# Optimization experiments

Measured on AMD Instinct MI355X. Metric: run time of the kernel, lower is better.

## Reference

```python
import jax, jax.numpy as jnp
import numpy as np
from jax import lax

B, T, L, OUT, SP, E, H = 128, 300, 28, 28, 7, 20, 256
W = T - L + 1          # 273 sliding windows
W_OUT = W - OUT        # 245 training windows
F_IN = L + 1 + E       # 49 rnn input features


def _lstm_dilated(x, d, Wih, Whh, b):
    # x: [T0, B, F]; dilation d realized by phase-stacking time into batch (zalando DRNN scheme)
    T0, Bn, F = x.shape
    pad = (-T0) % d
    if pad:
        x = jnp.concatenate([x, jnp.zeros((pad, Bn, F), x.dtype)], axis=0)
    Tn = x.shape[0] // d
    xd = x.reshape(Tn, d * Bn, F)  # element [k, j*Bn:(j+1)*Bn] == x[k*d+j]
    Hh = Whh.shape[1]

    def step(carry, xt):
        h, c = carry
        z = xt @ Wih.T + h @ Whh.T + b
        i, f, g, o = jnp.split(z, 4, axis=-1)  # torch LSTM gate order i,f,g,o
        c = jax.nn.sigmoid(f) * c + jax.nn.sigmoid(i) * jnp.tanh(g)
        h = jax.nn.sigmoid(o) * jnp.tanh(c)
        return (h, c), h

    h0 = jnp.zeros((d * Bn, Hh), x.dtype)
    _, hs = lax.scan(step, (h0, h0), xd)
    return hs.reshape(Tn * d, Bn, Hh)[:T0]


def _forward(train_dataset, val_dataset, alpha_raw, gamma_raw, init_seas,
             input_categories, my_param,
             Wih1, Whh1, b1, Wih2, Whh2, b2, Wih3, Whh3, b3, Wih4, Whh4, b4,
             linear_W, linear_b, score_W, score_b):
    x = train_dataset
    a = jax.nn.sigmoid(alpha_raw)   # [B]
    g = jax.nn.sigmoid(gamma_raw)   # [B]
    S0 = jnp.exp(init_seas)         # [B,7] = seasonalities[0..6]
    s7 = S0[:, 0]                   # seasonalities[7] = exp(init[:,0])
    level0 = x[:, 0] / S0[:, 0]
    buf0 = jnp.concatenate([S0[:, 1:], s7[:, None]], axis=1)  # S[1..7], shift register

    def es_step(carry, xt):
        level, buf = carry
        s = buf[:, 0]
        lvl = a * (xt / s) + (1.0 - a) * level
        s_new = g * (xt / lvl) + (1.0 - g) * s
        buf = jnp.concatenate([buf[:, 1:], s_new[:, None]], axis=1)
        return (lvl, buf), (lvl, s_new)

    _, (lvls, s_news) = lax.scan(es_step, (level0, buf0), x[:, 1:].T)
    levels = jnp.concatenate([level0[None], lvls], axis=0).T        # [B,T]
    S_full = jnp.concatenate([S0, s7[:, None], s_news.T], axis=1)   # [B,T+7]
    # extension: cat(S_full, S_full[:, T : T-7+28])  -> [B, T+28]
    S_ext = jnp.concatenate([S_full, S_full[:, T:T - SP + OUT]], axis=1)

    # input windows (vectorized over all W window positions)
    widx = jnp.arange(W)[:, None] + jnp.arange(L)[None, :]          # [W,L]
    lvl_w = levels[:, L - 1 + jnp.arange(W)]                        # [B,W]
    norm_in = x[:, widx] / S_ext[:, widx] / lvl_w[:, :, None]       # [B,W,L]
    cats = jnp.broadcast_to(input_categories[:, None, :], (B, W, E))
    cat_in = jnp.concatenate([norm_in, cats], axis=2)[jnp.arange(B) % 10]  # original j%10 row pick
    mp = jnp.broadcast_to(my_param.reshape(1, 1, 1), (B, W, 1))
    window_input = jnp.transpose(jnp.concatenate([cat_in, mp], axis=2), (1, 0, 2))  # [W,B,F_IN]

    # output windows
    oidx = (L + jnp.arange(W_OUT))[:, None] + jnp.arange(OUT)[None, :]  # [W_OUT,OUT]
    lvl_o = levels[:, L - 1 + jnp.arange(W_OUT)]                        # [B,W_OUT]
    window_output = jnp.transpose(x[:, oidx] / S_ext[:, oidx] / lvl_o[:, :, None], (1, 0, 2))

    # residual dilated LSTM stack: block1 dilations (1,2); block2 dilations (2,6) + residual
    h1 = _lstm_dilated(window_input, 1, Wih1, Whh1, b1)
    h1 = _lstm_dilated(h1, 2, Wih2, Whh2, b2)
    h2 = _lstm_dilated(h1, 2, Wih3, Whh3, b3)
    h2 = _lstm_dilated(h2, 6, Wih4, Whh4, b4) + h1
    h = jnp.tanh(h2 @ linear_W.T + linear_b)
    rnn_out = h @ score_W.T + score_b                                   # [W,B,OUT]

    # LSTM stack is causal, so running on window_input[:-OUT] equals slicing the full run
    prediction_values = rnn_out[:-OUT]
    actual_values = window_output
    holdout = rnn_out[-1] * S_ext[:, -OUT:] * levels[:, -1:]
    holdout_prediction = holdout * (holdout > 0).astype(holdout.dtype)
    hav = val_dataset
    hav_norm = hav / S_ext[:, -OUT:] / levels[:, -1:]
    return (prediction_values, actual_values, holdout_prediction, rnn_out, hav, hav_norm)


def setup_inputs() -> dict:
    key = jax.random.key(0)
    ks = jax.random.split(key, 24)
    s = float(1.0 / np.sqrt(H))
    u = lambda k, shape: jax.random.uniform(k, shape, jnp.float32, -s, s)
    inp = {
        "train_dataset": jax.random.uniform(ks[0], (B, T), jnp.float32) * 2.0 + 0.5,  # positive sales
        "val_dataset": jax.random.uniform(ks[1], (B, OUT), jnp.float32) * 2.0 + 0.5,
        "alpha_raw": jnp.full((B,), 0.5, jnp.float32),
        "gamma_raw": jnp.full((B,), 0.5, jnp.float32),
        "init_seas": jnp.full((B, SP), 0.5, jnp.float32),
        "input_categories": jnp.full((B, E), 0.001, jnp.float32) + 0.01 * jax.random.normal(ks[2], (B, E), jnp.float32),
        "my_param": jnp.full((1,), 0.001, jnp.float32),
        "Wih1": u(ks[3], (4 * H, F_IN)), "Whh1": u(ks[4], (4 * H, H)), "b1": u(ks[5], (4 * H,)),
        "Wih2": u(ks[6], (4 * H, H)), "Whh2": u(ks[7], (4 * H, H)), "b2": u(ks[8], (4 * H,)),
        "Wih3": u(ks[9], (4 * H, H)), "Whh3": u(ks[10], (4 * H, H)), "b3": u(ks[11], (4 * H,)),
        "Wih4": u(ks[12], (4 * H, H)), "Whh4": u(ks[13], (4 * H, H)), "b4": u(ks[14], (4 * H,)),
        "linear_W": u(ks[15], (H, H)), "linear_b": u(ks[16], (H,)),
        "score_W": u(ks[17], (OUT, H)), "score_b": u(ks[18], (OUT,)),
    }
    return inp


def reference(train_dataset, val_dataset, alpha_raw, gamma_raw, init_seas,
              input_categories, my_param,
              Wih1, Whh1, b1, Wih2, Whh2, b2, Wih3, Whh3, b3, Wih4, Whh4, b4,
              linear_W, linear_b, score_W, score_b):
    return _forward(train_dataset, val_dataset, alpha_raw, gamma_raw, init_seas,
                    input_categories, my_param,
                    Wih1, Whh1, b1, Wih2, Whh2, b2, Wih3, Whh3, b3, Wih4, Whh4, b4,
                    linear_W, linear_b, score_W, score_b)
```

## Files before the change

kernel.cpp:

```cpp
#include <hip/hip_runtime.h>

typedef unsigned short u16;
typedef unsigned int   u32;

static __device__ __forceinline__ float sigf (float x){ return 1.0f/(1.0f+__expf(-x)); }
static __device__ __forceinline__ float tanh_(float x){ return 2.0f/(1.0f+__expf(-2.0f*x)) - 1.0f; }

#define NM 2730
#define N_O0 878080
#define N_O3 978432

static __device__ __forceinline__ int dot4(u32 a, u32 b, int acc){
#if __has_builtin(__builtin_amdgcn_sdot4)
  return __builtin_amdgcn_sdot4((int)a, (int)b, acc, false);
#else
  int s = acc;
  #pragma unroll
  for(int i=0;i<4;i++){
    int av = (int)((signed char)((a >> (8*i)) & 0xffu));
    int bv = (int)((signed char)((b >> (8*i)) & 0xffu));
    s += av*bv;
  }
  return s;
#endif
}

__global__ __launch_bounds__(256) void k_prep(
    const float* __restrict__ x,     float* __restrict__ xT,
    const float* __restrict__ wi0,   float* __restrict__ wT0,
    const float* __restrict__ wi1,   float* __restrict__ wT1,
    const float* __restrict__ wi2,   float* __restrict__ wT2,
    const float* __restrict__ wi3,   float* __restrict__ wT3,
    const float* __restrict__ lw,    float* __restrict__ lwT,
    const float* __restrict__ sw,    float* __restrict__ swT,
    const float* __restrict__ h0, const float* __restrict__ h1,
    const float* __restrict__ h2, const float* __restrict__ h3,
    float* __restrict__ zsc){
  int i = blockIdx.x*256 + threadIdx.x;
  if(i < 38400){
    int t = i >> 7, b = i & 127;
    xT[i] = x[b*300 + t];
    return;
  }
  i -= 38400;
  if(i < 50176){ int c=i/1024, r=i-c*1024; wT0[i] = wi0[r*49 + c];  return; }
  i -= 50176;
  if(i < 262144){ int c=i>>10, r=i&1023; wT1[i] = wi1[r*256 + c];   return; }
  i -= 262144;
  if(i < 262144){ int c=i>>10, r=i&1023; wT2[i] = wi2[r*256 + c];   return; }
  i -= 262144;
  if(i < 262144){ int c=i>>10, r=i&1023; wT3[i] = wi3[r*256 + c];   return; }
  i -= 262144;
  if(i < 65536){ int c=i>>8, r=i&255; lwT[i] = lw[r*256 + c];       return; }
  i -= 65536;
  if(i < 7168){ int c=i/28, r=i-c*28; swT[i] = sw[r*256 + c];       return; }
  i -= 7168;
  if(i < 4096){
    int l = i >> 10, r = i & 1023;
    const float* W = (l==0)?h0:(l==1)?h1:(l==2)?h2:h3;
    const float4* p = (const float4*)(W + (size_t)r*256);
    float m = 0.f;
    #pragma unroll 8
    for(int q=0;q<64;q++){
      float4 v = p[q];
      m = fmaxf(m, fmaxf(fmaxf(fabsf(v.x),fabsf(v.y)), fmaxf(fabsf(v.z),fabsf(v.w))));
    }
    zsc[i] = fmaxf(m, 1e-20f) * (1.0f/16129.0f);
  }
}

__global__ __launch_bounds__(256) void k_packes(
    const float* __restrict__ h0, const float* __restrict__ h1,
    const float* __restrict__ h2, const float* __restrict__ h3,
    const float* __restrict__ zsc, u32* __restrict__ W8,
    const float* __restrict__ xT, const float* __restrict__ alpha,
    const float* __restrict__ gamma, const float* __restrict__ iseas,
    float* __restrict__ ST, float* __restrict__ lvlT){
  if(blockIdx.x < 1024){
    int i = blockIdx.x*256 + threadIdx.x;
    int l = i >> 16;
    int uidx = i & 65535;
    int dw = uidx & 3;
    int kg = (uidx >> 2) & 127;
    int q  = (uidx >> 9) & 3;
    int rr = (uidx >> 11) & 7;
    int js = uidx >> 14;
    int row = rr*128 + kg;
    int k0  = js*64 + q*16 + dw*4;
    const float* W = (l==0)?h0:(l==1)?h1:(l==2)?h2:h3;
    float inv = 1.0f / (zsc[l*1024 + row] * 127.0f);
    u32 out = 0;
    #pragma unroll
    for(int b=0;b<4;b++){
      float v = W[(size_t)row*256 + k0 + b];
      int q8 = max(-127, min(127, __float2int_rn(v * inv)));
      out |= ((u32)(q8 & 0xff)) << (8*b);
    }
    W8[i] = out;
    return;
  }
  int b = threadIdx.x;
  if(b >= 128) return;
  float a = sigf(alpha[b]);
  float g = sigf(gamma[b]);
  float S0[7];
  #pragma unroll
  for(int i=0;i<7;i++){ S0[i] = __expf(iseas[b*7+i]); ST[i*128+b] = S0[i]; }
  ST[7*128+b] = S0[0];
  float q0=S0[1],q1=S0[2],q2=S0[3],q3=S0[4],q4=S0[5],q5=S0[6],q6=S0[0];
  float lvl = xT[b]/S0[0];
  lvlT[b] = lvl;
  for(int t=1;t<300;t++){
    float xt = xT[t*128+b];
    float s  = q0;
    lvl = a*(xt/s) + (1.0f-a)*lvl;
    float sn = g*(xt/lvl) + (1.0f-g)*s;
    q0=q1;q1=q2;q2=q3;q3=q4;q4=q5;q5=q6;q6=sn;
    lvlT[t*128+b]   = lvl;
    ST[(t+7)*128+b] = sn;
  }
}

__global__ __launch_bounds__(256) void k_gemm1(
    const float* __restrict__ xT, const float* __restrict__ ST,
    const float* __restrict__ lvlT, const float* __restrict__ cats,
    const float* __restrict__ mp,
    const float* __restrict__ WT,
    const float* __restrict__ bias,
    float* __restrict__ Z){
  __shared__ float Xs[8][52];
  const int tid = threadIdx.x;
  const int m0 = blockIdx.x*8;
  for(int idx=tid; idx<8*49; idx+=256){
    int p = idx/49, f = idx - p*49;
    int m = m0+p;
    float v = 0.f;
    if(m < NM){
      int tt = m/10, jj = m - (m/10)*10;
      if(f < 28){
        int c = tt + f;
        v = xT[c*128 + jj] / ST[c*128 + jj] / lvlT[(tt+27)*128 + jj];
      } else if(f < 48){
        v = cats[jj*20 + (f-28)];
      } else {
        v = mp[0];
      }
    }
    Xs[p][f] = v;
  }
  __syncthreads();
  float acc0[8], acc1[8], acc2[8], acc3[8];
  {
    float b0 = bias[tid];
    float b1 = bias[tid+256];
    float b2 = bias[tid+512];
    float b3 = bias[tid+768];
    #pragma unroll
    for(int p=0;p<8;p++){ acc0[p]=b0; acc1[p]=b1; acc2[p]=b2; acc3[p]=b3; }
  }
  #pragma unroll 7
  for(int f=0; f<49; f++){
    float w0 = WT[f*1024 + tid      ];
    float w1 = WT[f*1024 + tid+256  ];
    float w2 = WT[f*1024 + tid+512  ];
    float w3 = WT[f*1024 + tid+768  ];
    #pragma unroll
    for(int p=0;p<8;p++){
      float xv = Xs[p][f];
      acc0[p] += w0*xv; acc1[p] += w1*xv; acc2[p] += w2*xv; acc3[p] += w3*xv;
    }
  }
  for(int p=0;p<8;p++){
    int m = m0+p;
    if(m < NM){
      float* zb = Z + m*1024 + tid;
      zb[0]=acc0[p]; zb[256]=acc1[p]; zb[512]=acc2[p]; zb[768]=acc3[p];
    }
  }
}

__global__ __launch_bounds__(256) void k_gemm(const float* __restrict__ X,
                                              const float* __restrict__ WT,
                                              const float* __restrict__ bias,
                                              float* __restrict__ Z){
  __shared__ float Xs[8][256];
  const int tid = threadIdx.x;
  const int m0 = blockIdx.x*8;
  for(int p=0;p<8;p++){
    int m = m0+p;
    Xs[p][tid] = (m < NM) ? X[m*256+tid] : 0.0f;
  }
  __syncthreads();
  float acc0[8], acc1[8], acc2[8], acc3[8];
  {
    float b0 = bias[tid];
    float b1 = bias[tid+256];
    float b2 = bias[tid+512];
    float b3 = bias[tid+768];
    #pragma unroll
    for(int p=0;p<8;p++){ acc0[p]=b0; acc1[p]=b1; acc2[p]=b2; acc3[p]=b3; }
  }
  #pragma unroll 4
  for(int f=0; f<256; f++){
    float w0 = WT[f*1024 + tid      ];
    float w1 = WT[f*1024 + tid+256  ];
    float w2 = WT[f*1024 + tid+512  ];
    float w3 = WT[f*1024 + tid+768  ];
    #pragma unroll
    for(int p=0;p<8;p++){
      float xv = Xs[p][f];
      acc0[p] += w0*xv; acc1[p] += w1*xv; acc2[p] += w2*xv; acc3[p] += w3*xv;
    }
  }
  for(int p=0;p<8;p++){
    int m = m0+p;
    if(m < NM){
      float* zb = Z + m*1024 + tid;
      zb[0]=acc0[p]; zb[256]=acc1[p]; zb[512]=acc2[p]; zb[768]=acc3[p];
    }
  }
}

__global__ __launch_bounds__(512) void k_scan8(
    const float* __restrict__ Z,
    const u32* __restrict__ W8,
    const float* __restrict__ zsc,
    float* __restrict__ Y,
    const float* __restrict__ RES,
    int d){
  __shared__ __align__(16) u32 h8[64];
  __shared__ int   zp[4][1024];
  __shared__ float sc[1024];
  __shared__ __align__(16) u32 wl[5*2048];
  const int tid = threadIdx.x;
  const int chain = blockIdx.x;
  const int j = chain % 10;
  const int r = chain / 10;
  const int ns = (273 - r + d - 1)/d;
  const int kg = tid & 127;
  const int js = tid >> 7;
  const uint4* Wb = (const uint4*)W8 + (size_t)js*4096 + kg;
  const uint4* hq = (const uint4*)h8 + js*4;
  uint4* wl4 = (uint4*)wl;

  for(int i=tid;i<1024;i+=512) sc[i] = zsc[i];
  #pragma unroll
  for(int rr=0;rr<5;rr++) wl4[rr*512 + tid] = Wb[rr*512];
  if(tid < 64) h8[tid] = 0u;
  float cst = 0.0f;
  __syncthreads();

  int t = r;
  for(int s=0; s<ns; s++, t+=d){
    const size_t row = (size_t)(t*10 + j);
    float zv0=0.f, zv1=0.f, zv2=0.f, zv3=0.f, rv=0.f;
    if(tid < 256){
      const float* zb = Z + row*1024;
      zv0 = zb[tid]; zv1 = zb[tid+256]; zv2 = zb[tid+512]; zv3 = zb[tid+768];
      if(RES) rv = RES[row*256 + tid];
    }
    int a0=0,a1=0,a2=0,a3=0,a4=0,a5=0,a6=0,a7=0;
    #pragma unroll
    for(int q=0;q<4;q++){
      uint4 h4 = hq[q];
      #pragma unroll
      for(int rr=0;rr<8;rr++){
        uint4 w = (q==0 && rr<5) ? wl4[rr*512 + tid] : Wb[rr*512 + q*128];
        int* ap = (rr==0)?&a0:(rr==1)?&a1:(rr==2)?&a2:(rr==3)?&a3:
                  (rr==4)?&a4:(rr==5)?&a5:(rr==6)?&a6:&a7;
        int acc = *ap;
        acc = dot4(w.x, h4.x, acc);
        acc = dot4(w.y, h4.y, acc);
        acc = dot4(w.z, h4.z, acc);
        acc = dot4(w.w, h4.w, acc);
        *ap = acc;
      }
    }
    zp[js][       kg] = a0;
    zp[js][128  + kg] = a1;
    zp[js][256  + kg] = a2;
    zp[js][384  + kg] = a3;
    zp[js][512  + kg] = a4;
    zp[js][640  + kg] = a5;
    zp[js][768  + kg] = a6;
    zp[js][896  + kg] = a7;
    __syncthreads();
    if(tid < 256){
      const int u = tid;
      int si = zp[0][u]     + zp[1][u]     + zp[2][u]     + zp[3][u];
      int sf = zp[0][u+256] + zp[1][u+256] + zp[2][u+256] + zp[3][u+256];
      int sg = zp[0][u+512] + zp[1][u+512] + zp[2][u+512] + zp[3][u+512];
      int so = zp[0][u+768] + zp[1][u+768] + zp[2][u+768] + zp[3][u+768];
      float zi = zv0 + sc[u]     * (float)si;
      float zf = zv1 + sc[u+256] * (float)sf;
      float zg = zv2 + sc[u+512] * (float)sg;
      float zo = zv3 + sc[u+768] * (float)so;
      float c  = sigf(zf)*cst + sigf(zi)*tanh_(zg);
      float h  = sigf(zo)*tanh_(c);
      cst = c;
      int hqi = __float2int_rn(h * 127.0f);
      hqi = max(-127, min(127, hqi));
      ((signed char*)h8)[u] = (signed char)hqi;
      Y[row*256 + u] = h + rv;
    }
    __syncthreads();
  }
}

__global__ __launch_bounds__(256) void k_headout(const float* __restrict__ Y4,
    const float* __restrict__ LWT,
    const float* __restrict__ lb,
    const float* __restrict__ SWT,
    const float* __restrict__ sb,
    const float* __restrict__ ST, const float* __restrict__ lvlT,
    const float* __restrict__ xT, const float* __restrict__ val,
    float* __restrict__ out){
  __shared__ float v [8][256];
  __shared__ float h2[8][256];
  const int tid = threadIdx.x;
  if(blockIdx.x >= 342){
    int i = (blockIdx.x - 342)*256 + tid;
    if(i < N_O0){
      int o = i % 28;
      int b = (i/28) % 128;
      int t = i/(28*128);
      int c = 28 + t + o;
      out[878080 + i] = xT[c*128+b] / ST[c*128+b] / lvlT[(27+t)*128+b];
    } else {
      i -= N_O0;
      if(i < 3584){
        int b = i/28, o = i%28;
        int col = (o < 21) ? (286+o) : (279+o);
        float Sm = ST[col*128 + b];
        float lv = lvlT[299*128 + b];
        out[2738176 + i] = val[i];
        out[2741760 + i] = val[i] / Sm / lv;
      }
    }
    return;
  }
  const int m0 = blockIdx.x*8;
  for(int p=0;p<8;p++){
    int m = m0+p;
    v[p][tid] = (m<NM) ? Y4[m*256+tid] : 0.0f;
  }
  __syncthreads();
  float acc[8];
  float bz = lb[tid];
  #pragma unroll
  for(int p=0;p<8;p++) acc[p]=bz;
  #pragma unroll 4
  for(int f=0; f<256; f++){
    float w = LWT[f*256+tid];
    #pragma unroll
    for(int p=0;p<8;p++) acc[p] += w * v[p][f];
  }
  #pragma unroll
  for(int p=0;p<8;p++) h2[p][tid] = tanh_(acc[p]);
  __syncthreads();
  if(tid < 224){
    int o = tid % 28, p = tid / 28;
    int m = m0 + p;
    if(m < NM){
      float a = sb[o];
      for(int f=0; f<256; f++) a += SWT[f*28+o] * h2[p][f];
      int t = m / 10, j = m - t*10;
      float* o0 = out;
      float* o3 = out + 1759744;
      for(int b=j; b<128; b+=10){
        size_t idx = (size_t)t*3584 + b*28 + o;
        o3[idx] = a;
        if(t < 245) o0[idx] = a;
      }
      if(t == 272){
        int col = (o < 21) ? (286+o) : (279+o);
        float* o2 = out + 1756160;
        for(int b=j; b<128; b+=10){
          float hv = a * ST[col*128 + b] * lvlT[299*128 + b];
          o2[b*28 + o] = (hv > 0.0f) ? hv : 0.0f;
        }
      }
    }
  }
}

extern "C" void kernel_launch(void* const* d_in, const int* in_sizes, int n_in,
                              void* d_out, int out_size, void* d_ws, size_t ws_size,
                              hipStream_t stream){
  (void)in_sizes; (void)n_in; (void)out_size; (void)ws_size;
  const float* x     = (const float*)d_in[0];
  const float* val   = (const float*)d_in[1];
  const float* alpha = (const float*)d_in[2];
  const float* gamma = (const float*)d_in[3];
  const float* iseas = (const float*)d_in[4];
  const float* cats  = (const float*)d_in[5];
  const float* mp    = (const float*)d_in[6];
  const float* Wih[4]  = {(const float*)d_in[7],  (const float*)d_in[10], (const float*)d_in[13], (const float*)d_in[16]};
  const float* Whh[4]  = {(const float*)d_in[8],  (const float*)d_in[11], (const float*)d_in[14], (const float*)d_in[17]};
  const float* bias[4] = {(const float*)d_in[9],  (const float*)d_in[12], (const float*)d_in[15], (const float*)d_in[18]};
  const float* linW  = (const float*)d_in[19];
  const float* linb  = (const float*)d_in[20];
  const float* scW   = (const float*)d_in[21];
  const float* scb   = (const float*)d_in[22];

  float* Fw   = (float*)d_ws;
  float* ST   = Fw;
  float* lvlT = ST   + 39296;
  float* xT   = lvlT + 38400;
  float* xz   = xT   + 38400;
  float* yA   = xz   + 2795520;
  float* yB   = yA   + 698880;
  float* wihT[4];
  wihT[0] = yB + 698880;
  wihT[1] = wihT[0] + 50176;
  wihT[2] = wihT[1] + 262144;
  wihT[3] = wihT[2] + 262144;
  float* linWT = wihT[3] + 262144;
  float* scT   = linWT + 65536;
  float* zsc   = scT   + 7168;
  u32*   W8all = (u32*)(zsc + 4096);

  k_prep<<<3718, 256, 0, stream>>>(x, xT,
      Wih[0], wihT[0], Wih[1], wihT[1], Wih[2], wihT[2], Wih[3], wihT[3],
      linW, linWT, scW, scT,
      Whh[0], Whh[1], Whh[2], Whh[3], zsc);

  k_packes<<<1025, 256, 0, stream>>>(Whh[0], Whh[1], Whh[2], Whh[3], zsc, W8all,
                                     xT, alpha, gamma, iseas, ST, lvlT);

  const int    dlt[4]    = {1, 2, 2, 6};
  const int    chains[4] = {10, 20, 20, 60};
  const float* Xin[4]    = {nullptr, yA, yB, yA};
  float*       Yout[4]   = {yA, yB, yA, yA};
  for(int l=0;l<4;l++){
    if(l == 0)
      k_gemm1<<<(NM+7)/8, 256, 0, stream>>>(xT, ST, lvlT, cats, mp,
                                            wihT[0], bias[0], xz);
    else
      k_gemm<<<(NM+7)/8, 256, 0, stream>>>(Xin[l], wihT[l], bias[l], xz);
    k_scan8<<<chains[l], 512, 0, stream>>>(xz, W8all + l*65536, zsc + l*1024,
                                           Yout[l],
                                           (l==3) ? yB : (const float*)nullptr, dlt[l]);
  }

  k_headout<<<342 + (N_O0 + 3584 + 255)/256, 256, 0, stream>>>(
      yA, linWT, linb, scT, scb, ST, lvlT, xT, val, (float*)d_out);
}
```

Measured before the change: 1.037 ms.

## Restructure recurrent scan to one gate row per thread with 1024 threads

The int8 recurrent matvec is remapped so each of 1024 threads computes one full gate row over all 256 hidden inputs. This removes the cross-thread partial-sum reduction through shared memory and one barrier's worth of work. The weight packing layout changes to match: 9 of the 16 k-chunks stay resident in LDS (144KB), and the other 7 are reloaded from global or L2 into registers every step. The trailing __syncthreads is replaced with a raw s_waitcnt/s_barrier, which adds register pressure and makes correctness depend on that inline asm.

```diff
diff --git a/kernel.cpp b/kernel.cpp
--- a/kernel.cpp
+++ b/kernel.cpp
@@ -79,14 +79,11 @@
   if(blockIdx.x < 1024){
     int i = blockIdx.x*256 + threadIdx.x;
     int l = i >> 16;
-    int uidx = i & 65535;
-    int dw = uidx & 3;
-    int kg = (uidx >> 2) & 127;
-    int q  = (uidx >> 9) & 3;
-    int rr = (uidx >> 11) & 7;
-    int js = uidx >> 14;
-    int row = rr*128 + kg;
-    int k0  = js*64 + q*16 + dw*4;
+    int p = i & 65535;
+    int dw  = p & 3;
+    int row = (p >> 2) & 1023;
+    int iw  = p >> 12;
+    int k0  = iw*16 + dw*4;
     const float* W = (l==0)?h0:(l==1)?h1:(l==2)?h2:h3;
     float inv = 1.0f / (zsc[l*1024 + row] * 127.0f);
     u32 out = 0;
@@ -221,31 +218,28 @@
   }
 }
 
-__global__ __launch_bounds__(512) void k_scan8(
+__global__ __launch_bounds__(1024) void k_scan8(
     const float* __restrict__ Z,
     const u32* __restrict__ W8,
     const float* __restrict__ zsc,
     float* __restrict__ Y,
     const float* __restrict__ RES,
     int d){
+  __shared__ __align__(16) u32 wl[9*4096];
   __shared__ __align__(16) u32 h8[64];
-  __shared__ int   zp[4][1024];
-  __shared__ float sc[1024];
-  __shared__ __align__(16) u32 wl[5*2048];
+  __shared__ float zf[1024];
   const int tid = threadIdx.x;
   const int chain = blockIdx.x;
   const int j = chain % 10;
   const int r = chain / 10;
   const int ns = (273 - r + d - 1)/d;
-  const int kg = tid & 127;
-  const int js = tid >> 7;
-  const uint4* Wb = (const uint4*)W8 + (size_t)js*4096 + kg;
-  const uint4* hq = (const uint4*)h8 + js*4;
+  const uint4* Wc = (const uint4*)W8;
   uint4* wl4 = (uint4*)wl;
-
-  for(int i=tid;i<1024;i+=512) sc[i] = zsc[i];
+  const uint4* hq = (const uint4*)h8;
+
   #pragma unroll
-  for(int rr=0;rr<5;rr++) wl4[rr*512 + tid] = Wb[rr*512];
+  for(int i=0;i<9;i++) wl4[i*1024 + tid] = Wc[i*1024 + tid];
+  const float sct = zsc[tid];
   if(tid < 64) h8[tid] = 0u;
   float cst = 0.0f;
   __syncthreads();
@@ -253,49 +247,53 @@
   int t = r;
   for(int s=0; s<ns; s++, t+=d){
     const size_t row = (size_t)(t*10 + j);
-    float zv0=0.f, zv1=0.f, zv2=0.f, zv3=0.f, rv=0.f;
-    if(tid < 256){
-      const float* zb = Z + row*1024;
-      zv0 = zb[tid]; zv1 = zb[tid+256]; zv2 = zb[tid+512]; zv3 = zb[tid+768];
-      if(RES) rv = RES[row*256 + tid];
-    }
-    int a0=0,a1=0,a2=0,a3=0,a4=0,a5=0,a6=0,a7=0;
-    #pragma unroll
-    for(int q=0;q<4;q++){
-      uint4 h4 = hq[q];
-      #pragma unroll
-      for(int rr=0;rr<8;rr++){
-        uint4 w = (q==0 && rr<5) ? wl4[rr*512 + tid] : Wb[rr*512 + q*128];
-        int* ap = (rr==0)?&a0:(rr==1)?&a1:(rr==2)?&a2:(rr==3)?&a3:
-                  (rr==4)?&a4:(rr==5)?&a5:(rr==6)?&a6:&a7;
-        int acc = *ap;
-        acc = dot4(w.x, h4.x, acc);
-        acc = dot4(w.y, h4.y, acc);
-        acc = dot4(w.z, h4.z, acc);
-        acc = dot4(w.w, h4.w, acc);
-        *ap = acc;
-      }
-    }
-    zp[js][       kg] = a0;
-    zp[js][128  + kg] = a1;
-    zp[js][256  + kg] = a2;
-    zp[js][384  + kg] = a3;
-    zp[js][512  + kg] = a4;
-    zp[js][640  + kg] = a5;
-    zp[js][768  + kg] = a6;
-    zp[js][896  + kg] = a7;
+    uint4 ws0 = Wc[ 9*1024 + tid];
+    uint4 ws1 = Wc[10*1024 + tid];
+    uint4 ws2 = Wc[11*1024 + tid];
+    uint4 ws3 = Wc[12*1024 + tid];
+    uint4 ws4 = Wc[13*1024 + tid];
+    uint4 ws5 = Wc[14*1024 + tid];
+    uint4 ws6 = Wc[15*1024 + tid];
+    float zv = Z[row*1024 + tid];
+    float rv = 0.f;
+    if(RES && tid < 256) rv = RES[row*256 + tid];
+
+    int acc = 0;
+    #pragma unroll
+    for(int i=0;i<9;i++){
+      uint4 w  = wl4[i*1024 + tid];
+      uint4 h4 = hq[i];
+      acc = dot4(w.x, h4.x, acc);
+      acc = dot4(w.y, h4.y, acc);
+      acc = dot4(w.z, h4.z, acc);
+      acc = dot4(w.w, h4.w, acc);
+    }
+    {
+      uint4 h4;
+      h4 = hq[ 9]; acc = dot4(ws0.x,h4.x,acc); acc = dot4(ws0.y,h4.y,acc);
+                   acc = dot4(ws0.z,h4.z,acc); acc = dot4(ws0.w,h4.w,acc);
+      h4 = hq[10]; acc = dot4(ws1.x,h4.x,acc); acc = dot4(ws1.y,h4.y,acc);
+                   acc = dot4(ws1.z,h4.z,acc); acc = dot4(ws1.w,h4.w,acc);
+      h4 = hq[11]; acc = dot4(ws2.x,h4.x,acc); acc = dot4(ws2.y,h4.y,acc);
+                   acc = dot4(ws2.z,h4.z,acc); acc = dot4(ws2.w,h4.w,acc);
+      h4 = hq[12]; acc = dot4(ws3.x,h4.x,acc); acc = dot4(ws3.y,h4.y,acc);
+                   acc = dot4(ws3.z,h4.z,acc); acc = dot4(ws3.w,h4.w,acc);
+      h4 = hq[13]; acc = dot4(ws4.x,h4.x,acc); acc = dot4(ws4.y,h4.y,acc);
+                   acc = dot4(ws4.z,h4.z,acc); acc = dot4(ws4.w,h4.w,acc);
+      h4 = hq[14]; acc = dot4(ws5.x,h4.x,acc); acc = dot4(ws5.y,h4.y,acc);
+                   acc = dot4(ws5.z,h4.z,acc); acc = dot4(ws5.w,h4.w,acc);
+      h4 = hq[15]; acc = dot4(ws6.x,h4.x,acc); acc = dot4(ws6.y,h4.y,acc);
+                   acc = dot4(ws6.z,h4.z,acc); acc = dot4(ws6.w,h4.w,acc);
+    }
+    zf[tid] = zv + sct * (float)acc;
     __syncthreads();
     if(tid < 256){
       const int u = tid;
-      int si = zp[0][u]     + zp[1][u]     + zp[2][u]     + zp[3][u];
-      int sf = zp[0][u+256] + zp[1][u+256] + zp[2][u+256] + zp[3][u+256];
-      int sg = zp[0][u+512] + zp[1][u+512] + zp[2][u+512] + zp[3][u+512];
-      int so = zp[0][u+768] + zp[1][u+768] + zp[2][u+768] + zp[3][u+768];
-      float zi = zv0 + sc[u]     * (float)si;
-      float zf = zv1 + sc[u+256] * (float)sf;
-      float zg = zv2 + sc[u+512] * (float)sg;
-      float zo = zv3 + sc[u+768] * (float)so;
-      float c  = sigf(zf)*cst + sigf(zi)*tanh_(zg);
+      float zi = zf[u];
+      float zff= zf[u+256];
+      float zg = zf[u+512];
+      float zo = zf[u+768];
+      float c  = sigf(zff)*cst + sigf(zi)*tanh_(zg);
       float h  = sigf(zo)*tanh_(c);
       cst = c;
       int hqi = __float2int_rn(h * 127.0f);
@@ -303,7 +301,7 @@
       ((signed char*)h8)[u] = (signed char)hqi;
       Y[row*256 + u] = h + rv;
     }
-    __syncthreads();
+    asm volatile("s_waitcnt lgkmcnt(0)\n\ts_barrier" ::: "memory");
   }
 }
 
@@ -438,9 +436,9 @@
                                             wihT[0], bias[0], xz);
     else
       k_gemm<<<(NM+7)/8, 256, 0, stream>>>(Xin[l], wihT[l], bias[l], xz);
-    k_scan8<<<chains[l], 512, 0, stream>>>(xz, W8all + l*65536, zsc + l*1024,
-                                           Yout[l],
-                                           (l==3) ? yB : (const float*)nullptr, dlt[l]);
+    k_scan8<<<chains[l], 1024, 0, stream>>>(xz, W8all + l*65536, zsc + l*1024,
+                                            Yout[l],
+                                            (l==3) ? yB : (const float*)nullptr, dlt[l]);
   }
 
   k_headout<<<342 + (N_O0 + 3584 + 255)/256, 256, 0, stream>>>(
```

After: 1.104 ms. 1.07x slower.

## Fuse all stages into one cooperative persistent kernel with grid syncs

Applied to the files above, without the earlier changes.

Replaces the sequence of prep, pack, gemm, scan and head kernel launches with a single cooperative kernel of 256 blocks that runs every stage and uses grid-wide barriers between them. It also drops the LDS-cached weight preload in the scan and loads the ES input series into shared memory for the serial smoothing loop. The aim is to remove the launch and inter-kernel gaps across the many small stages. In exchange, the gemm stages run on only 256 blocks with 512 threads using a single large static LDS buffer, so occupancy and gemm throughput may drop, and grid sync has its own cost.

```diff
diff --git a/kernel.cpp b/kernel.cpp
--- a/kernel.cpp
+++ b/kernel.cpp
@@ -1,14 +1,14 @@
 #include <hip/hip_runtime.h>
-
-typedef unsigned short u16;
-typedef unsigned int   u32;
+#include <hip/hip_cooperative_groups.h>
+namespace cg = cooperative_groups;
+
+typedef unsigned int u32;
 
 static __device__ __forceinline__ float sigf (float x){ return 1.0f/(1.0f+__expf(-x)); }
 static __device__ __forceinline__ float tanh_(float x){ return 2.0f/(1.0f+__expf(-2.0f*x)) - 1.0f; }
 
 #define NM 2730
 #define N_O0 878080
-#define N_O3 978432
 
 static __device__ __forceinline__ int dot4(u32 a, u32 b, int acc){
 #if __has_builtin(__builtin_amdgcn_sdot4)
@@ -25,227 +25,100 @@
 #endif
 }
 
-__global__ __launch_bounds__(256) void k_prep(
-    const float* __restrict__ x,     float* __restrict__ xT,
-    const float* __restrict__ wi0,   float* __restrict__ wT0,
-    const float* __restrict__ wi1,   float* __restrict__ wT1,
-    const float* __restrict__ wi2,   float* __restrict__ wT2,
-    const float* __restrict__ wi3,   float* __restrict__ wT3,
-    const float* __restrict__ lw,    float* __restrict__ lwT,
-    const float* __restrict__ sw,    float* __restrict__ swT,
-    const float* __restrict__ h0, const float* __restrict__ h1,
-    const float* __restrict__ h2, const float* __restrict__ h3,
-    float* __restrict__ zsc){
-  int i = blockIdx.x*256 + threadIdx.x;
-  if(i < 38400){
-    int t = i >> 7, b = i & 127;
-    xT[i] = x[b*300 + t];
-    return;
-  }
-  i -= 38400;
-  if(i < 50176){ int c=i/1024, r=i-c*1024; wT0[i] = wi0[r*49 + c];  return; }
-  i -= 50176;
-  if(i < 262144){ int c=i>>10, r=i&1023; wT1[i] = wi1[r*256 + c];   return; }
-  i -= 262144;
-  if(i < 262144){ int c=i>>10, r=i&1023; wT2[i] = wi2[r*256 + c];   return; }
-  i -= 262144;
-  if(i < 262144){ int c=i>>10, r=i&1023; wT3[i] = wi3[r*256 + c];   return; }
-  i -= 262144;
-  if(i < 65536){ int c=i>>8, r=i&255; lwT[i] = lw[r*256 + c];       return; }
-  i -= 65536;
-  if(i < 7168){ int c=i/28, r=i-c*28; swT[i] = sw[r*256 + c];       return; }
-  i -= 7168;
-  if(i < 4096){
-    int l = i >> 10, r = i & 1023;
-    const float* W = (l==0)?h0:(l==1)?h1:(l==2)?h2:h3;
-    const float4* p = (const float4*)(W + (size_t)r*256);
-    float m = 0.f;
-    #pragma unroll 8
-    for(int q=0;q<64;q++){
-      float4 v = p[q];
-      m = fmaxf(m, fmaxf(fmaxf(fabsf(v.x),fabsf(v.y)), fmaxf(fabsf(v.z),fabsf(v.w))));
-    }
-    zsc[i] = fmaxf(m, 1e-20f) * (1.0f/16129.0f);
-  }
-}
-
-__global__ __launch_bounds__(256) void k_packes(
-    const float* __restrict__ h0, const float* __restrict__ h1,
-    const float* __restrict__ h2, const float* __restrict__ h3,
-    const float* __restrict__ zsc, u32* __restrict__ W8,
-    const float* __restrict__ xT, const float* __restrict__ alpha,
-    const float* __restrict__ gamma, const float* __restrict__ iseas,
-    float* __restrict__ ST, float* __restrict__ lvlT){
-  if(blockIdx.x < 1024){
-    int i = blockIdx.x*256 + threadIdx.x;
-    int l = i >> 16;
-    int uidx = i & 65535;
-    int dw = uidx & 3;
-    int kg = (uidx >> 2) & 127;
-    int q  = (uidx >> 9) & 3;
-    int rr = (uidx >> 11) & 7;
-    int js = uidx >> 14;
-    int row = rr*128 + kg;
-    int k0  = js*64 + q*16 + dw*4;
-    const float* W = (l==0)?h0:(l==1)?h1:(l==2)?h2:h3;
-    float inv = 1.0f / (zsc[l*1024 + row] * 127.0f);
-    u32 out = 0;
-    #pragma unroll
-    for(int b=0;b<4;b++){
-      float v = W[(size_t)row*256 + k0 + b];
-      int q8 = max(-127, min(127, __float2int_rn(v * inv)));
-      out |= ((u32)(q8 & 0xff)) << (8*b);
-    }
-    W8[i] = out;
-    return;
-  }
-  int b = threadIdx.x;
-  if(b >= 128) return;
-  float a = sigf(alpha[b]);
-  float g = sigf(gamma[b]);
-  float S0[7];
-  #pragma unroll
-  for(int i=0;i<7;i++){ S0[i] = __expf(iseas[b*7+i]); ST[i*128+b] = S0[i]; }
-  ST[7*128+b] = S0[0];
-  float q0=S0[1],q1=S0[2],q2=S0[3],q3=S0[4],q4=S0[5],q5=S0[6],q6=S0[0];
-  float lvl = xT[b]/S0[0];
-  lvlT[b] = lvl;
-  for(int t=1;t<300;t++){
-    float xt = xT[t*128+b];
-    float s  = q0;
-    lvl = a*(xt/s) + (1.0f-a)*lvl;
-    float sn = g*(xt/lvl) + (1.0f-g)*s;
-    q0=q1;q1=q2;q2=q3;q3=q4;q4=q5;q5=q6;q6=sn;
-    lvlT[t*128+b]   = lvl;
-    ST[(t+7)*128+b] = sn;
-  }
-}
-
-__global__ __launch_bounds__(256) void k_gemm1(
-    const float* __restrict__ xT, const float* __restrict__ ST,
-    const float* __restrict__ lvlT, const float* __restrict__ cats,
-    const float* __restrict__ mp,
-    const float* __restrict__ WT,
-    const float* __restrict__ bias,
-    float* __restrict__ Z){
-  __shared__ float Xs[8][52];
+struct MegaArgs {
+  const float *x, *val, *alpha, *gamma, *iseas, *cats, *mp;
+  const float *wi0, *wi1, *wi2, *wi3;
+  const float *hh0, *hh1, *hh2, *hh3;
+  const float *bs0, *bs1, *bs2, *bs3;
+  const float *linW, *linb, *scW, *scb;
+  float *out;
+  float *ST, *lvlT, *xT, *xz, *yA, *yB;
+  float *wT0, *wT1, *wT2, *wT3, *linWT, *scT, *zsc;
+  u32   *W8;
+};
+
+template<bool FIRST>
+__device__ __forceinline__ void gemm_body(const MegaArgs& A, char* smem,
+    const float* X, const float* WT, const float* bias, float* Z){
   const int tid = threadIdx.x;
-  const int m0 = blockIdx.x*8;
-  for(int idx=tid; idx<8*49; idx+=256){
-    int p = idx/49, f = idx - p*49;
-    int m = m0+p;
-    float v = 0.f;
-    if(m < NM){
-      int tt = m/10, jj = m - (m/10)*10;
-      if(f < 28){
-        int c = tt + f;
-        v = xT[c*128 + jj] / ST[c*128 + jj] / lvlT[(tt+27)*128 + jj];
-      } else if(f < 48){
-        v = cats[jj*20 + (f-28)];
-      } else {
-        v = mp[0];
-      }
-    }
-    Xs[p][f] = v;
-  }
-  __syncthreads();
-  float acc0[8], acc1[8], acc2[8], acc3[8];
-  {
-    float b0 = bias[tid];
-    float b1 = bias[tid+256];
-    float b2 = bias[tid+512];
-    float b3 = bias[tid+768];
-    #pragma unroll
-    for(int p=0;p<8;p++){ acc0[p]=b0; acc1[p]=b1; acc2[p]=b2; acc3[p]=b3; }
-  }
-  #pragma unroll 7
-  for(int f=0; f<49; f++){
-    float w0 = WT[f*1024 + tid      ];
-    float w1 = WT[f*1024 + tid+256  ];
-    float w2 = WT[f*1024 + tid+512  ];
-    float w3 = WT[f*1024 + tid+768  ];
-    #pragma unroll
+  const int bid = blockIdx.x;
+  constexpr int K    = FIRST ? 49 : 256;
+  constexpr int XSTR = FIRST ? 52 : 256;
+  float* Xs = (float*)smem;
+  for(int vb = bid; vb < 342; vb += 256){
+    const int m0 = vb*8;
+    if(FIRST){
+      for(int idx=tid; idx<8*49; idx+=512){
+        int p = idx/49, f = idx - p*49;
+        int m = m0 + p;
+        float v = 0.f;
+        if(m < NM){
+          int tt = m/10, jj = m - (m/10)*10;
+          if(f < 28){
+            int c = tt + f;
+            v = A.xT[c*128+jj] / A.ST[c*128+jj] / A.lvlT[(tt+27)*128+jj];
+          } else if(f < 48){
+            v = A.cats[jj*20 + (f-28)];
+          } else {
+            v = A.mp[0];
+          }
+        }
+        Xs[p*XSTR + f] = v;
+      }
+    } else {
+      for(int idx=tid; idx<2048; idx+=512){
+        int p = idx >> 8, c = idx & 255;
+        int m = m0 + p;
+        Xs[p*XSTR + c] = (m < NM) ? X[(size_t)m*256 + c] : 0.f;
+      }
+    }
+    __syncthreads();
+    float a0[8], a1[8];
+    {
+      float b0 = bias[tid], b1 = bias[tid+512];
+      #pragma unroll
+      for(int p=0;p<8;p++){ a0[p]=b0; a1[p]=b1; }
+    }
+    #pragma unroll 7
+    for(int f=0; f<K; f++){
+      float w0 = WT[f*1024 + tid];
+      float w1 = WT[f*1024 + tid + 512];
+      #pragma unroll
+      for(int p=0;p<8;p++){
+        float xv = Xs[p*XSTR + f];
+        a0[p] += w0*xv; a1[p] += w1*xv;
+      }
+    }
     for(int p=0;p<8;p++){
-      float xv = Xs[p][f];
-      acc0[p] += w0*xv; acc1[p] += w1*xv; acc2[p] += w2*xv; acc3[p] += w3*xv;
-    }
-  }
-  for(int p=0;p<8;p++){
-    int m = m0+p;
-    if(m < NM){
-      float* zb = Z + m*1024 + tid;
-      zb[0]=acc0[p]; zb[256]=acc1[p]; zb[512]=acc2[p]; zb[768]=acc3[p];
-    }
-  }
-}
-
-__global__ __launch_bounds__(256) void k_gemm(const float* __restrict__ X,
-                                              const float* __restrict__ WT,
-                                              const float* __restrict__ bias,
-                                              float* __restrict__ Z){
-  __shared__ float Xs[8][256];
+      int m = m0 + p;
+      if(m < NM){
+        float* zb = Z + (size_t)m*1024;
+        zb[tid] = a0[p]; zb[tid+512] = a1[p];
+      }
+    }
+    __syncthreads();
+  }
+}
+
+__device__ __forceinline__ void scan_body(const MegaArgs& A, char* smem,
+    int layer, int chains, int d, const float* Z, float* Y, const float* RES){
   const int tid = threadIdx.x;
-  const int m0 = blockIdx.x*8;
-  for(int p=0;p<8;p++){
-    int m = m0+p;
-    Xs[p][tid] = (m < NM) ? X[m*256+tid] : 0.0f;
-  }
-  __syncthreads();
-  float acc0[8], acc1[8], acc2[8], acc3[8];
-  {
-    float b0 = bias[tid];
-    float b1 = bias[tid+256];
-    float b2 = bias[tid+512];
-    float b3 = bias[tid+768];
-    #pragma unroll
-    for(int p=0;p<8;p++){ acc0[p]=b0; acc1[p]=b1; acc2[p]=b2; acc3[p]=b3; }
-  }
-  #pragma unroll 4
-  for(int f=0; f<256; f++){
-    float w0 = WT[f*1024 + tid      ];
-    float w1 = WT[f*1024 + tid+256  ];
-    float w2 = WT[f*1024 + tid+512  ];
-    float w3 = WT[f*1024 + tid+768  ];
-    #pragma unroll
-    for(int p=0;p<8;p++){
-      float xv = Xs[p][f];
-      acc0[p] += w0*xv; acc1[p] += w1*xv; acc2[p] += w2*xv; acc3[p] += w3*xv;
-    }
-  }
-  for(int p=0;p<8;p++){
-    int m = m0+p;
-    if(m < NM){
-      float* zb = Z + m*1024 + tid;
-      zb[0]=acc0[p]; zb[256]=acc1[p]; zb[512]=acc2[p]; zb[768]=acc3[p];
-    }
-  }
-}
-
-__global__ __launch_bounds__(512) void k_scan8(
-    const float* __restrict__ Z,
-    const u32* __restrict__ W8,
-    const float* __restrict__ zsc,
-    float* __restrict__ Y,
-    const float* __restrict__ RES,
-    int d){
-  __shared__ __align__(16) u32 h8[64];
-  __shared__ int   zp[4][1024];
-  __shared__ float sc[1024];
-  __shared__ __align__(16) u32 wl[5*2048];
-  const int tid = threadIdx.x;
-  const int chain = blockIdx.x;
-  const int j = chain % 10;
-  const int r = chain / 10;
+  const int bid = blockIdx.x;
+  if(bid >= chains) return;
+  u32*   h8 = (u32*)smem;
+  int*   zp = (int*)(smem + 256);
+  float* sc = (float*)(smem + 256 + 16384);
+  const u32* W8 = A.W8 + (size_t)layer*65536;
+  const float* zsc = A.zsc + layer*1024;
+  const int j = bid % 10;
+  const int r = bid / 10;
   const int ns = (273 - r + d - 1)/d;
   const int kg = tid & 127;
   const int js = tid >> 7;
   const uint4* Wb = (const uint4*)W8 + (size_t)js*4096 + kg;
   const uint4* hq = (const uint4*)h8 + js*4;
-  uint4* wl4 = (uint4*)wl;
 
   for(int i=tid;i<1024;i+=512) sc[i] = zsc[i];
-  #pragma unroll
-  for(int rr=0;rr<5;rr++) wl4[rr*512 + tid] = Wb[rr*512];
   if(tid < 64) h8[tid] = 0u;
   float cst = 0.0f;
   __syncthreads();
@@ -265,7 +138,7 @@
       uint4 h4 = hq[q];
       #pragma unroll
       for(int rr=0;rr<8;rr++){
-        uint4 w = (q==0 && rr<5) ? wl4[rr*512 + tid] : Wb[rr*512 + q*128];
+        uint4 w = Wb[rr*512 + q*128];
         int* ap = (rr==0)?&a0:(rr==1)?&a1:(rr==2)?&a2:(rr==3)?&a3:
                   (rr==4)?&a4:(rr==5)?&a5:(rr==6)?&a6:&a7;
         int acc = *ap;
@@ -276,21 +149,21 @@
         *ap = acc;
       }
     }
-    zp[js][       kg] = a0;
-    zp[js][128  + kg] = a1;
-    zp[js][256  + kg] = a2;
-    zp[js][384  + kg] = a3;
-    zp[js][512  + kg] = a4;
-    zp[js][640  + kg] = a5;
-    zp[js][768  + kg] = a6;
-    zp[js][896  + kg] = a7;
+    zp[js*1024 +       kg] = a0;
+    zp[js*1024 + 128 + kg] = a1;
+    zp[js*1024 + 256 + kg] = a2;
+    zp[js*1024 + 384 + kg] = a3;
+    zp[js*1024 + 512 + kg] = a4;
+    zp[js*1024 + 640 + kg] = a5;
+    zp[js*1024 + 768 + kg] = a6;
+    zp[js*1024 + 896 + kg] = a7;
     __syncthreads();
     if(tid < 256){
       const int u = tid;
-      int si = zp[0][u]     + zp[1][u]     + zp[2][u]     + zp[3][u];
-      int sf = zp[0][u+256] + zp[1][u+256] + zp[2][u+256] + zp[3][u+256];
-      int sg = zp[0][u+512] + zp[1][u+512] + zp[2][u+512] + zp[3][u+512];
-      int so = zp[0][u+768] + zp[1][u+768] + zp[2][u+768] + zp[3][u+768];
+      int si = zp[u]        + zp[1024+u]     + zp[2048+u]     + zp[3072+u];
+      int sf = zp[u+256]    + zp[1024+u+256] + zp[2048+u+256] + zp[3072+u+256];
+      int sg = zp[u+512]    + zp[1024+u+512] + zp[2048+u+512] + zp[3072+u+512];
+      int so = zp[u+768]    + zp[1024+u+768] + zp[2048+u+768] + zp[3072+u+768];
       float zi = zv0 + sc[u]     * (float)si;
       float zf = zv1 + sc[u+256] * (float)sf;
       float zg = zv2 + sc[u+512] * (float)sg;
@@ -303,146 +176,219 @@
       ((signed char*)h8)[u] = (signed char)hqi;
       Y[row*256 + u] = h + rv;
     }
+    asm volatile("s_waitcnt lgkmcnt(0)\n\ts_barrier" ::: "memory");
+  }
+}
+
+__global__ __launch_bounds__(512) void k_mega(MegaArgs A){
+  __shared__ __align__(16) char smem[153600];
+  const int tid = threadIdx.x;
+  const int bid = blockIdx.x;
+  cg::grid_group gg = cg::this_grid();
+  #define GSYNC() do{ __threadfence(); gg.sync(); __threadfence(); }while(0)
+
+  for(int i0 = bid*512 + tid; i0 < 951808; i0 += 131072){
+    int i = i0;
+    if(i < 38400){ int t=i>>7, b=i&127; A.xT[i] = A.x[b*300+t]; }
+    else { i -= 38400;
+    if(i < 50176){ int c=i/1024, r=i-c*1024; A.wT0[i] = A.wi0[r*49+c]; }
+    else { i -= 50176;
+    if(i < 262144){ int c=i>>10, r=i&1023; A.wT1[i] = A.wi1[r*256+c]; }
+    else { i -= 262144;
+    if(i < 262144){ int c=i>>10, r=i&1023; A.wT2[i] = A.wi2[r*256+c]; }
+    else { i -= 262144;
+    if(i < 262144){ int c=i>>10, r=i&1023; A.wT3[i] = A.wi3[r*256+c]; }
+    else { i -= 262144;
+    if(i < 65536){ int c=i>>8, r=i&255; A.linWT[i] = A.linW[r*256+c]; }
+    else { i -= 65536;
+    if(i < 7168){ int c=i/28, r=i-c*28; A.scT[i] = A.scW[r*256+c]; }
+    else { i -= 7168;
+    if(i < 4096){
+      int l = i >> 10, r = i & 1023;
+      const float* W = (l==0)?A.hh0:(l==1)?A.hh1:(l==2)?A.hh2:A.hh3;
+      const float4* p4 = (const float4*)(W + (size_t)r*256);
+      float m = 0.f;
+      #pragma unroll 8
+      for(int q=0;q<64;q++){
+        float4 v = p4[q];
+        m = fmaxf(m, fmaxf(fmaxf(fabsf(v.x),fabsf(v.y)), fmaxf(fabsf(v.z),fabsf(v.w))));
+      }
+      A.zsc[i] = fmaxf(m, 1e-20f) * (1.0f/16129.0f);
+    }}}}}}}}
+  }
+  GSYNC();
+
+  for(int i = bid*512 + tid; i < 262144; i += 131072){
+    int l = i >> 16;
+    int uidx = i & 65535;
+    int dw = uidx & 3;
+    int kg = (uidx >> 2) & 127;
+    int q  = (uidx >> 9) & 3;
+    int rr = (uidx >> 11) & 7;
+    int js = uidx >> 14;
+    int row = rr*128 + kg;
+    int k0  = js*64 + q*16 + dw*4;
+    const float* W = (l==0)?A.hh0:(l==1)?A.hh1:(l==2)?A.hh2:A.hh3;
+    float inv = 1.0f / (A.zsc[l*1024 + row] * 127.0f);
+    u32 outv = 0;
+    #pragma unroll
+    for(int b=0;b<4;b++){
+      float v = W[(size_t)row*256 + k0 + b];
+      int q8 = max(-127, min(127, __float2int_rn(v * inv)));
+      outv |= ((u32)(q8 & 0xff)) << (8*b);
+    }
+    A.W8[i] = outv;
+  }
+  if(bid == 0){
+    float* xs = (float*)smem;
+    for(int i=tid; i<38400; i+=512) xs[i] = A.xT[i];
     __syncthreads();
-  }
-}
-
-__global__ __launch_bounds__(256) void k_headout(const float* __restrict__ Y4,
-    const float* __restrict__ LWT,
-    const float* __restrict__ lb,
-    const float* __restrict__ SWT,
-    const float* __restrict__ sb,
-    const float* __restrict__ ST, const float* __restrict__ lvlT,
-    const float* __restrict__ xT, const float* __restrict__ val,
-    float* __restrict__ out){
-  __shared__ float v [8][256];
-  __shared__ float h2[8][256];
-  const int tid = threadIdx.x;
-  if(blockIdx.x >= 342){
-    int i = (blockIdx.x - 342)*256 + tid;
+    if(tid < 128){
+      int b = tid;
+      float av = sigf(A.alpha[b]);
+      float gv = sigf(A.gamma[b]);
+      float S0[7];
+      #pragma unroll
+      for(int i=0;i<7;i++){ S0[i] = __expf(A.iseas[b*7+i]); A.ST[i*128+b] = S0[i]; }
+      A.ST[7*128+b] = S0[0];
+      float q0=S0[1],q1=S0[2],q2=S0[3],q3=S0[4],q4=S0[5],q5=S0[6],q6=S0[0];
+      float lvl = xs[b]/S0[0];
+      A.lvlT[b] = lvl;
+      for(int t=1;t<300;t++){
+        float xt = xs[t*128+b];
+        float s  = q0;
+        lvl = av*(xt/s) + (1.0f-av)*lvl;
+        float sn = gv*(xt/lvl) + (1.0f-gv)*s;
+        q0=q1;q1=q2;q2=q3;q3=q4;q4=q5;q5=q6;q6=sn;
+        A.lvlT[t*128+b]   = lvl;
+        A.ST[(t+7)*128+b] = sn;
+      }
+    }
+  }
+  GSYNC();
+
+  gemm_body<true >(A, smem, nullptr, A.wT0, A.bs0, A.xz);  GSYNC();
+  scan_body(A, smem, 0, 10, 1, A.xz, A.yA, nullptr);       GSYNC();
+  gemm_body<false>(A, smem, A.yA, A.wT1, A.bs1, A.xz);     GSYNC();
+  scan_body(A, smem, 1, 20, 2, A.xz, A.yB, nullptr);       GSYNC();
+  gemm_body<false>(A, smem, A.yB, A.wT2, A.bs2, A.xz);     GSYNC();
+  scan_body(A, smem, 2, 20, 2, A.xz, A.yA, nullptr);       GSYNC();
+  gemm_body<false>(A, smem, A.yA, A.wT3, A.bs3, A.xz);     GSYNC();
+  scan_body(A, smem, 3, 60, 6, A.xz, A.yA, A.yB);          GSYNC();
+
+  {
+    float* v  = (float*)smem;
+    float* h2 = v + 2048;
+    for(int vb = bid; vb < 342; vb += 256){
+      const int m0 = vb*8;
+      for(int idx=tid; idx<2048; idx+=512){
+        int p = idx >> 8, c = idx & 255;
+        int m = m0 + p;
+        v[p*256+c] = (m < NM) ? A.yA[(size_t)m*256+c] : 0.f;
+      }
+      __syncthreads();
+      if(tid < 256){
+        float acc[8];
+        float bz = A.linb[tid];
+        #pragma unroll
+        for(int p=0;p<8;p++) acc[p] = bz;
+        #pragma unroll 4
+        for(int f=0; f<256; f++){
+          float w = A.linWT[f*256+tid];
+          #pragma unroll
+          for(int p=0;p<8;p++) acc[p] += w * v[p*256+f];
+        }
+        #pragma unroll
+        for(int p=0;p<8;p++) h2[p*256+tid] = tanh_(acc[p]);
+      }
+      __syncthreads();
+      if(tid < 224){
+        int o = tid % 28, p = tid / 28;
+        int m = m0 + p;
+        if(m < NM){
+          float a = A.scb[o];
+          for(int f=0; f<256; f++) a += A.scT[f*28+o] * h2[p*256+f];
+          int t = m / 10, j = m - t*10;
+          float* o0 = A.out;
+          float* o3 = A.out + 1759744;
+          for(int b=j; b<128; b+=10){
+            size_t idx = (size_t)t*3584 + b*28 + o;
+            o3[idx] = a;
+            if(t < 245) o0[idx] = a;
+          }
+          if(t == 272){
+            int col = (o < 21) ? (286+o) : (279+o);
+            float* o2 = A.out + 1756160;
+            for(int b=j; b<128; b+=10){
+              float hv = a * A.ST[col*128 + b] * A.lvlT[299*128 + b];
+              o2[b*28 + o] = (hv > 0.0f) ? hv : 0.0f;
+            }
+          }
+        }
+      }
+      __syncthreads();
+    }
+  }
+  for(int i0 = bid*512 + tid; i0 < N_O0 + 3584; i0 += 131072){
+    int i = i0;
     if(i < N_O0){
       int o = i % 28;
       int b = (i/28) % 128;
       int t = i/(28*128);
       int c = 28 + t + o;
-      out[878080 + i] = xT[c*128+b] / ST[c*128+b] / lvlT[(27+t)*128+b];
+      A.out[878080 + i] = A.xT[c*128+b] / A.ST[c*128+b] / A.lvlT[(27+t)*128+b];
     } else {
       i -= N_O0;
-      if(i < 3584){
-        int b = i/28, o = i%28;
-        int col = (o < 21) ? (286+o) : (279+o);
-        float Sm = ST[col*128 + b];
-        float lv = lvlT[299*128 + b];
-        out[2738176 + i] = val[i];
-        out[2741760 + i] = val[i] / Sm / lv;
-      }
-    }
-    return;
-  }
-  const int m0 = blockIdx.x*8;
-  for(int p=0;p<8;p++){
-    int m = m0+p;
-    v[p][tid] = (m<NM) ? Y4[m*256+tid] : 0.0f;
-  }
-  __syncthreads();
-  float acc[8];
-  float bz = lb[tid];
-  #pragma unroll
-  for(int p=0;p<8;p++) acc[p]=bz;
-  #pragma unroll 4
-  for(int f=0; f<256; f++){
-    float w = LWT[f*256+tid];
-    #pragma unroll
-    for(int p=0;p<8;p++) acc[p] += w * v[p][f];
-  }
-  #pragma unroll
-  for(int p=0;p<8;p++) h2[p][tid] = tanh_(acc[p]);
-  __syncthreads();
-  if(tid < 224){
-    int o = tid % 28, p = tid / 28;
-    int m = m0 + p;
-    if(m < NM){
-      float a = sb[o];
-      for(int f=0; f<256; f++) a += SWT[f*28+o] * h2[p][f];
-      int t = m / 10, j = m - t*10;
-      float* o0 = out;
-      float* o3 = out + 1759744;
-      for(int b=j; b<128; b+=10){
-        size_t idx = (size_t)t*3584 + b*28 + o;
-        o3[idx] = a;
-        if(t < 245) o0[idx] = a;
-      }
-      if(t == 272){
-        int col = (o < 21) ? (286+o) : (279+o);
-        float* o2 = out + 1756160;
-        for(int b=j; b<128; b+=10){
-          float hv = a * ST[col*128 + b] * lvlT[299*128 + b];
-          o2[b*28 + o] = (hv > 0.0f) ? hv : 0.0f;
-        }
-      }
-    }
-  }
+      int b = i/28, o = i%28;
+      int col = (o < 21) ? (286+o) : (279+o);
+      float Sm = A.ST[col*128 + b];
+      float lv = A.lvlT[299*128 + b];
+      A.out[2738176 + i] = A.val[i];
+      A.out[2741760 + i] = A.val[i] / Sm / lv;
+    }
+  }
+  #undef GSYNC
 }
 
 extern "C" void kernel_launch(void* const* d_in, const int* in_sizes, int n_in,
                               void* d_out, int out_size, void* d_ws, size_t ws_size,
                               hipStream_t stream){
   (void)in_sizes; (void)n_in; (void)out_size; (void)ws_size;
-  const float* x     = (const float*)d_in[0];
-  const float* val   = (const float*)d_in[1];
-  const float* alpha = (const float*)d_in[2];
-  const float* gamma = (const float*)d_in[3];
-  const float* iseas = (const float*)d_in[4];
-  const float* cats  = (const float*)d_in[5];
-  const float* mp    = (const float*)d_in[6];
-  const float* Wih[4]  = {(const float*)d_in[7],  (const float*)d_in[10], (const float*)d_in[13], (const float*)d_in[16]};
-  const float* Whh[4]  = {(const float*)d_in[8],  (const float*)d_in[11], (const float*)d_in[14], (const float*)d_in[17]};
-  const float* bias[4] = {(const float*)d_in[9],  (const float*)d_in[12], (const float*)d_in[15], (const float*)d_in[18]};
-  const float* linW  = (const float*)d_in[19];
-  const float* linb  = (const float*)d_in[20];
-  const float* scW   = (const float*)d_in[21];
-  const float* scb   = (const float*)d_in[22];
-
-  float* Fw   = (float*)d_ws;
-  float* ST   = Fw;
-  float* lvlT = ST   + 39296;
-  float* xT   = lvlT + 38400;
-  float* xz   = xT   + 38400;
-  float* yA   = xz   + 2795520;
-  float* yB   = yA   + 698880;
-  float* wihT[4];
-  wihT[0] = yB + 698880;
-  wihT[1] = wihT[0] + 50176;
-  wihT[2] = wihT[1] + 262144;
-  wihT[3] = wihT[2] + 262144;
-  float* linWT = wihT[3] + 262144;
-  float* scT   = linWT + 65536;
-  float* zsc   = scT   + 7168;
-  u32*   W8all = (u32*)(zsc + 4096);
-
-  k_prep<<<3718, 256, 0, stream>>>(x, xT,
-      Wih[0], wihT[0], Wih[1], wihT[1], Wih[2], wihT[2], Wih[3], wihT[3],
-      linW, linWT, scW, scT,
-      Whh[0], Whh[1], Whh[2], Whh[3], zsc);
-
-  k_packes<<<1025, 256, 0, stream>>>(Whh[0], Whh[1], Whh[2], Whh[3], zsc, W8all,
-                                     xT, alpha, gamma, iseas, ST, lvlT);
-
-  const int    dlt[4]    = {1, 2, 2, 6};
-  const int    chains[4] = {10, 20, 20, 60};
-  const float* Xin[4]    = {nullptr, yA, yB, yA};
-  float*       Yout[4]   = {yA, yB, yA, yA};
-  for(int l=0;l<4;l++){
-    if(l == 0)
-      k_gemm1<<<(NM+7)/8, 256, 0, stream>>>(xT, ST, lvlT, cats, mp,
-                                            wihT[0], bias[0], xz);
-    else
-      k_gemm<<<(NM+7)/8, 256, 0, stream>>>(Xin[l], wihT[l], bias[l], xz);
-    k_scan8<<<chains[l], 512, 0, stream>>>(xz, W8all + l*65536, zsc + l*1024,
-                                           Yout[l],
-                                           (l==3) ? yB : (const float*)nullptr, dlt[l]);
-  }
-
-  k_headout<<<342 + (N_O0 + 3584 + 255)/256, 256, 0, stream>>>(
-      yA, linWT, linb, scT, scb, ST, lvlT, xT, val, (float*)d_out);
-}
+  MegaArgs A;
+  A.x     = (const float*)d_in[0];
+  A.val   = (const float*)d_in[1];
+  A.alpha = (const float*)d_in[2];
+  A.gamma = (const float*)d_in[3];
+  A.iseas = (const float*)d_in[4];
+  A.cats  = (const float*)d_in[5];
+  A.mp    = (const float*)d_in[6];
+  A.wi0 = (const float*)d_in[7];  A.hh0 = (const float*)d_in[8];  A.bs0 = (const float*)d_in[9];
+  A.wi1 = (const float*)d_in[10]; A.hh1 = (const float*)d_in[11]; A.bs1 = (const float*)d_in[12];
+  A.wi2 = (const float*)d_in[13]; A.hh2 = (const float*)d_in[14]; A.bs2 = (const float*)d_in[15];
+  A.wi3 = (const float*)d_in[16]; A.hh3 = (const float*)d_in[17]; A.bs3 = (const float*)d_in[18];
+  A.linW = (const float*)d_in[19];
+  A.linb = (const float*)d_in[20];
+  A.scW  = (const float*)d_in[21];
+  A.scb  = (const float*)d_in[22];
+  A.out  = (float*)d_out;
+
+  float* Fw = (float*)d_ws;
+  A.ST    = Fw;
+  A.lvlT  = A.ST   + 39296;
+  A.xT    = A.lvlT + 38400;
+  A.xz    = A.xT   + 38400;
+  A.yA    = A.xz   + 2795520;
+  A.yB    = A.yA   + 698880;
+  A.wT0   = A.yB   + 698880;
+  A.wT1   = A.wT0  + 50176;
+  A.wT2   = A.wT1  + 262144;
+  A.wT3   = A.wT2  + 262144;
+  A.linWT = A.wT3  + 262144;
+  A.scT   = A.linWT+ 65536;
+  A.zsc   = A.scT  + 7168;
+  A.W8    = (u32*)(A.zsc + 4096);
+
+  void* kargs[] = { (void*)&A };
+  hipLaunchCooperativeKernel((const void*)k_mega, dim3(256), dim3(512),
+                             kargs, 0, stream);
+}
```

Result: slower. 2.869 ms (+176.8%).
